# Optimization experiments

Measured on AMD Instinct MI355X. Metric: run time of the kernel, lower is better.

## Reference

```python
import jax, jax.numpy as jnp
import numpy as np

L, B, S, H, V = 6, 8, 2048, 768, 32000
FF = 4 * H
EPS = 1e-5


def _ln(x, g, b):
    m = x.mean(-1, keepdims=True)
    v = ((x - m) ** 2).mean(-1, keepdims=True)
    return (x - m) / jnp.sqrt(v + EPS) * g + b


def setup_inputs() -> dict:
    key = jax.random.key(0)
    ks = iter(jax.random.split(key, 32))
    std = 0.02
    n = lambda shape: jax.random.normal(next(ks), shape, dtype=jnp.float32) * std
    inp = {
        'input_ids': jax.random.randint(next(ks), (B, S), 0, V, dtype=jnp.int64),
        'attention_mask': jnp.ones((B, S), dtype=jnp.int32),
        'tok_emb': n((V, H)),
        'pos_emb': n((S, H)),
        'Wq': n((L, H, H)), 'bq': n((L, H)),
        'Wk': n((L, H, H)), 'bk': n((L, H)),
        'Wv': n((L, H, H)), 'bv': n((L, H)),
        'Wo': n((L, H, H)), 'bo': n((L, H)),
        'ln1_g': jnp.ones((L, H), jnp.float32), 'ln1_b': jnp.zeros((L, H), jnp.float32),
        'ln2_g': jnp.ones((L, H), jnp.float32), 'ln2_b': jnp.zeros((L, H), jnp.float32),
        'W1': n((L, H, FF)), 'b1': n((L, FF)),
        'W2': n((L, FF, H)), 'b2': n((L, H)),
        'fln_g': jnp.ones((H,), jnp.float32), 'fln_b': jnp.zeros((H,), jnp.float32),
        'cls_W': n((H, 1)), 'cls_b': n((1,)),
    }
    return inp


def reference(input_ids, attention_mask, tok_emb, pos_emb, Wq, bq, Wk, bk, Wv, bv,
              Wo, bo, ln1_g, ln1_b, ln2_g, ln2_b, W1, b1, W2, b2,
              fln_g, fln_b, cls_W, cls_b):
    x = tok_emb[input_ids] + pos_emb[None, :S, :]  # [B,S,H]
    causal = jnp.triu(jnp.ones((S, S), dtype=bool), 1)  # True above diagonal
    pad = ~(attention_mask.astype(bool))[:, None, :]    # [B,1,S] True where padded
    full_mask = causal[None, :, :] | pad                # [B,S,S]
    scale = 1.0 / (H ** 0.5)
    for i in range(L):
        # --- attention block (pre-LN) ---
        h = _ln(x, ln1_g[i], ln1_b[i])
        q = h @ Wq[i] + bq[i]
        k = h @ Wk[i] + bk[i]
        v = h @ Wv[i] + bv[i]
        scores = jnp.einsum('bqd,bkd->bqk', q, k) * scale
        scores = jnp.where(full_mask, -jnp.inf, scores)
        attn = jax.nn.softmax(scores, axis=-1)
        o = jnp.einsum('bqk,bkd->bqd', attn, v) @ Wo[i] + bo[i]
        x = o + x
        # --- FFN block ---
        h = _ln(x, ln2_g[i], ln2_b[i])
        x = jax.nn.gelu(h @ W1[i] + b1[i], approximate=False) @ W2[i] + b2[i] + x
    x = _ln(x, fln_g, fln_b)
    # select hidden state of last non-padded token per row
    m = attention_mask.astype(jnp.int32)
    last = m.sum(1) - 1                      # [B]
    x_last = x[jnp.arange(B), last]          # [B,H]
    logits = x_last @ cls_W + cls_b          # [B,1]
    return logits
```

## Files before the change

kernel.cpp:

```cpp
#include <hip/hip_runtime.h>
#include <hip/hip_bf16.h>

#define Bn 8
#define Sn 2048
#define Hn 768
#define FFn 3072
#define Ln 6
#define BSn (Bn * Sn)
#define CQ 512
#define LN_EPS 1e-5f

typedef __hip_bfloat16 bf16;
typedef __bf16 bf16x8 __attribute__((ext_vector_type(8)));
typedef float f32x4 __attribute__((ext_vector_type(4)));

__device__ __forceinline__ float b2f(bf16 v) { return __bfloat162float(v); }
__device__ __forceinline__ void stc(float* p, float v) { *p = v; }
__device__ __forceinline__ void stc(bf16* p, float v) { *p = __float2bfloat16(v); }

union Pk8 { float4 v; bf16 h[8]; };

__device__ __forceinline__ void gld16(const bf16* g, short* l) {
  __builtin_amdgcn_global_load_lds(
      (const __attribute__((address_space(1))) unsigned int*)g,
      (__attribute__((address_space(3))) unsigned int*)l, 16, 0, 0);
}

__global__ void __launch_bounds__(256) embed_kernel(
    const int* __restrict__ ids, const float* __restrict__ tok,
    const float* __restrict__ pos, float* __restrict__ x) {
  long t = blockIdx.x;
  int s = (int)(t & (Sn - 1));
  long id = ids[t];
  const float* tr = tok + id * Hn;
  const float* pr = pos + (long)s * Hn;
  float* xr = x + t * Hn;
  for (int d = threadIdx.x; d < Hn; d += 256)
    xr[d] = tr[d] + pr[d];
}

__global__ void __launch_bounds__(256) transpose_all_kernel(
    const float* __restrict__ Wq_l, const float* __restrict__ Wk_l,
    const float* __restrict__ Wv_l, const float* __restrict__ Wo_l,
    const float* __restrict__ W1_l, const float* __restrict__ W2_l,
    bf16* __restrict__ wt) {
  int id = blockIdx.x;
  const float* W;
  bf16* Wt;
  int K, N, tile, tilesX;
  if (id < 2304) {
    int w = id / 576;
    tile = id - w * 576;
    W = (w == 0) ? Wq_l : (w == 1) ? Wk_l : (w == 2) ? Wv_l : Wo_l;
    Wt = wt + (size_t)w * Hn * Hn;
    K = Hn; N = Hn; tilesX = Hn / 32;
  } else if (id < 4608) {
    tile = id - 2304;
    W = W1_l;
    Wt = wt + 4 * (size_t)Hn * Hn;
    K = Hn; N = FFn; tilesX = FFn / 32;
  } else {
    tile = id - 4608;
    W = W2_l;
    Wt = wt + 4 * (size_t)Hn * Hn + (size_t)Hn * FFn;
    K = FFn; N = Hn; tilesX = Hn / 32;
  }
  int n0 = (tile % tilesX) * 32, k0 = (tile / tilesX) * 32;

  __shared__ float t[32][33];
  int tx = threadIdx.x & 31, ty = threadIdx.x >> 5;
#pragma unroll
  for (int i = 0; i < 32; i += 8)
    t[ty + i][tx] = W[(long)(k0 + ty + i) * N + n0 + tx];
  __syncthreads();
#pragma unroll
  for (int i = 0; i < 32; i += 8)
    stc(Wt + (long)(n0 + ty + i) * K + k0 + tx, t[tx][ty + i]);
}

__global__ void __launch_bounds__(256) ln_kernel(
    const float* __restrict__ x, const float* __restrict__ g,
    const float* __restrict__ b, bf16* __restrict__ out) {
  long token = blockIdx.x;
  const float* xr = x + token * Hn;
  bf16* orow = out + token * Hn;
  int tid = threadIdx.x;

  float vals[3];
  float s1 = 0.f;
#pragma unroll
  for (int i = 0; i < 3; i++) {
    vals[i] = xr[tid + 256 * i];
    s1 += vals[i];
  }
  __shared__ float sb[4];
  __shared__ float stat[2];
#pragma unroll
  for (int off = 32; off > 0; off >>= 1) s1 += __shfl_down(s1, off, 64);
  if ((tid & 63) == 0) sb[tid >> 6] = s1;
  __syncthreads();
  if (tid == 0) stat[0] = (sb[0] + sb[1] + sb[2] + sb[3]) * (1.0f / Hn);
  __syncthreads();
  float mean = stat[0];

  float s2 = 0.f;
#pragma unroll
  for (int i = 0; i < 3; i++) {
    float d = vals[i] - mean;
    s2 += d * d;
  }
#pragma unroll
  for (int off = 32; off > 0; off >>= 1) s2 += __shfl_down(s2, off, 64);
  if ((tid & 63) == 0) sb[tid >> 6] = s2;
  __syncthreads();
  if (tid == 0)
    stat[1] = rsqrtf((sb[0] + sb[1] + sb[2] + sb[3]) * (1.0f / Hn) + LN_EPS);
  __syncthreads();
  float inv = stat[1];

#pragma unroll
  for (int i = 0; i < 3; i++) {
    int d = tid + 256 * i;
    stc(orow + d, (vals[i] - mean) * inv * g[d] + b[d]);
  }
}

template <int EPI, typename CT>
__global__ void __launch_bounds__(256) mfma_gemm_kernel(
    const bf16* __restrict__ A, const bf16* __restrict__ Bt,
    const float* __restrict__ bias, const float* __restrict__ res,
    CT* __restrict__ C, int M, int N, int K,
    const float* __restrict__ bias2, const float* __restrict__ bias3) {
  __shared__ short As[128 * 32];
  __shared__ short Bs[128 * 32];
  int tid = threadIdx.x;
  int wave = tid >> 6, lane = tid & 63;
  int waveM = wave >> 1, waveN = wave & 1;
  int quad = lane >> 4, l16 = lane & 15;

  int nwg = gridDim.x;
  int orig = blockIdx.x;
  int q8 = nwg >> 3, r8 = nwg & 7;
  int xcd = orig & 7, loc = orig >> 3;
  int wg = (xcd < r8 ? xcd * (q8 + 1) : r8 * (q8 + 1) + (xcd - r8) * q8) + loc;
  int gx = N >> 7;
  long colBase = (long)(wg % gx) * 128;
  long rowBase = (long)(wg / gx) * 128;

  const bf16* Ag = A + rowBase * K;
  const bf16* Bg = Bt + colBase * K;

  int srow = lane >> 2;
  int schunk = (lane & 3) * 8;

  f32x4 acc[4][4] = {};

  for (int kt = 0; kt < K; kt += 32) {
#pragma unroll
    for (int c = 0; c < 2; c++) {
      int r0 = wave * 32 + c * 16;
      gld16(Ag + (long)(r0 + srow) * K + kt + schunk, &As[r0 * 32]);
      gld16(Bg + (long)(r0 + srow) * K + kt + schunk, &Bs[r0 * 32]);
    }
    __syncthreads();

    bf16x8 af[4], bfr[4];
#pragma unroll
    for (int t = 0; t < 4; t++)
      af[t] = *(const bf16x8*)&As[(waveM * 64 + t * 16 + l16) * 32 + quad * 8];
#pragma unroll
    for (int u = 0; u < 4; u++)
      bfr[u] = *(const bf16x8*)&Bs[(waveN * 64 + u * 16 + l16) * 32 + quad * 8];
#pragma unroll
    for (int t = 0; t < 4; t++)
#pragma unroll
      for (int u = 0; u < 4; u++)
        acc[t][u] = __builtin_amdgcn_mfma_f32_16x16x32_bf16(af[t], bfr[u],
                                                            acc[t][u], 0, 0, 0);
    __syncthreads();
  }

#pragma unroll
  for (int t = 0; t < 4; t++) {
#pragma unroll
    for (int u = 0; u < 4; u++) {
      int col = (int)colBase + waveN * 64 + u * 16 + l16;
      if (EPI == 4) {
        long row0 = rowBase + waveM * 64 + t * 16 + quad * 4;
        if (col < 1536) {
          float bv = col < 768 ? bias[col] : bias2[col - 768];
          bf16* dst = (bf16*)C + (col < 768 ? 0 : (size_t)BSn * Hn - Hn);
#pragma unroll
          for (int r = 0; r < 4; r++)
            stc(dst + (row0 + r) * Hn + col, acc[t][u][r] + bv);
        } else {
          int vcol = col - 1536;
          float bv = bias3[vcol];
          union { uint2 w; bf16 h[4]; } pk;
          long bb = row0 >> 11;
          long s = row0 & (Sn - 1);
#pragma unroll
          for (int r = 0; r < 4; r++)
            pk.h[r] = __float2bfloat16(acc[t][u][r] + bv);
          bf16* vT = (bf16*)C + 2 * (size_t)BSn * Hn;
          *reinterpret_cast<uint2*>(vT + (bb * Hn + vcol) * Sn + s) = pk.w;
        }
      } else {
        float bv = bias[col];
#pragma unroll
        for (int r = 0; r < 4; r++) {
          long row = rowBase + waveM * 64 + t * 16 + quad * 4 + r;
          float v = acc[t][u][r] + bv;
          if (EPI == 1) v += res[row * N + col];
          if (EPI == 2) v = 0.5f * v * (1.0f + erff(v * 0.70710678118654752f));
          stc(C + row * N + col, v);
        }
      }
    }
  }
}

__global__ void __launch_bounds__(256) qk_mfma_kernel(
    const bf16* __restrict__ q, const bf16* __restrict__ k,
    bf16* __restrict__ sc, int q0) {
  int kBase = blockIdx.x * 128;
  int qBase = q0 + blockIdx.y * 128;
  if (kBase > qBase + 127) return;
  int b = blockIdx.z;
  const bf16* Ag = q + ((long)b * Sn + qBase) * Hn;
  const bf16* Bg = k + ((long)b * Sn + kBase) * Hn;

  __shared__ short As[128 * 32];
  __shared__ short Bs[128 * 32];
  int tid = threadIdx.x;
  int wave = tid >> 6, lane = tid & 63;
  int waveM = wave >> 1, waveN = wave & 1;
  int quad = lane >> 4, l16 = lane & 15;
  int srow = lane >> 2;
  int schunk = (lane & 3) * 8;

  f32x4 acc[4][4] = {};

  for (int kt = 0; kt < Hn; kt += 32) {
#pragma unroll
    for (int c = 0; c < 2; c++) {
      int r0 = wave * 32 + c * 16;
      gld16(Ag + (long)(r0 + srow) * Hn + kt + schunk, &As[r0 * 32]);
      gld16(Bg + (long)(r0 + srow) * Hn + kt + schunk, &Bs[r0 * 32]);
    }
    __syncthreads();

    bf16x8 af[4], bfr[4];
#pragma unroll
    for (int t = 0; t < 4; t++)
      af[t] = *(const bf16x8*)&As[(waveM * 64 + t * 16 + l16) * 32 + quad * 8];
#pragma unroll
    for (int u = 0; u < 4; u++)
      bfr[u] = *(const bf16x8*)&Bs[(waveN * 64 + u * 16 + l16) * 32 + quad * 8];
#pragma unroll
    for (int t = 0; t < 4; t++)
#pragma unroll
      for (int u = 0; u < 4; u++)
        acc[t][u] = __builtin_amdgcn_mfma_f32_16x16x32_bf16(af[t], bfr[u],
                                                            acc[t][u], 0, 0, 0);
    __syncthreads();
  }

  const float scale = 0.03608439182435161f;
#pragma unroll
  for (int t = 0; t < 4; t++)
#pragma unroll
    for (int u = 0; u < 4; u++) {
      int col = kBase + waveN * 64 + u * 16 + l16;
#pragma unroll
      for (int r = 0; r < 4; r++) {
        long qRel = (long)(qBase - q0) + waveM * 64 + t * 16 + quad * 4 + r;
        stc(sc + ((long)b * CQ + qRel) * Sn + col, acc[t][u][r] * scale);
      }
    }
}

__global__ void __launch_bounds__(256) pv_mfma_kernel(
    const bf16* __restrict__ p, const bf16* __restrict__ vT,
    bf16* __restrict__ o, int q0) {
  int colBase = blockIdx.x * 128;
  int qBase = q0 + blockIdx.y * 128;
  int b = blockIdx.z;
  int klimit = qBase + 128;
  const bf16* Ag = p + ((long)b * CQ + (qBase - q0)) * Sn;
  const bf16* Bg = vT + ((long)b * Hn + colBase) * Sn;

  __shared__ short As[128 * 32];
  __shared__ short Bs[128 * 32];
  int tid = threadIdx.x;
  int wave = tid >> 6, lane = tid & 63;
  int waveM = wave >> 1, waveN = wave & 1;
  int quad = lane >> 4, l16 = lane & 15;
  int srow = lane >> 2;
  int schunk = (lane & 3) * 8;

  f32x4 acc[4][4] = {};

  for (int kt = 0; kt < klimit; kt += 32) {
#pragma unroll
    for (int c = 0; c < 2; c++) {
      int r0 = wave * 32 + c * 16;
      gld16(Ag + (long)(r0 + srow) * Sn + kt + schunk, &As[r0 * 32]);
      gld16(Bg + (long)(r0 + srow) * Sn + kt + schunk, &Bs[r0 * 32]);
    }
    __syncthreads();

    bf16x8 af[4], bfr[4];
#pragma unroll
    for (int t = 0; t < 4; t++)
      af[t] = *(const bf16x8*)&As[(waveM * 64 + t * 16 + l16) * 32 + quad * 8];
#pragma unroll
    for (int u = 0; u < 4; u++)
      bfr[u] = *(const bf16x8*)&Bs[(waveN * 64 + u * 16 + l16) * 32 + quad * 8];
#pragma unroll
    for (int t = 0; t < 4; t++)
#pragma unroll
      for (int u = 0; u < 4; u++)
        acc[t][u] = __builtin_amdgcn_mfma_f32_16x16x32_bf16(af[t], bfr[u],
                                                            acc[t][u], 0, 0, 0);
    __syncthreads();
  }

#pragma unroll
  for (int t = 0; t < 4; t++)
#pragma unroll
    for (int u = 0; u < 4; u++) {
      int col = colBase + waveN * 64 + u * 16 + l16;
#pragma unroll
      for (int r = 0; r < 4; r++) {
        long qAbs = (long)qBase + waveM * 64 + t * 16 + quad * 4 + r;
        stc(o + ((long)b * Sn + qAbs) * Hn + col, acc[t][u][r]);
      }
    }
}

__global__ void __launch_bounds__(256) softmax_kernel(
    bf16* __restrict__ sc, const int* __restrict__ mask, int q0) {
  int qRel = blockIdx.x;
  int b = blockIdx.y;
  int qg = q0 + qRel;
  bf16* row = sc + ((long)b * CQ + qRel) * Sn;
  const int* mrow = mask + b * Sn;
  int tid = threadIdx.x;
  int n = qg + 1;
  int limit = (qg & ~127) + 128;
  int k0 = tid * 8;

  Pk8 pk;
  pk.v = *reinterpret_cast<const float4*>(row + k0);
  int4 m0 = *reinterpret_cast<const int4*>(mrow + k0);
  int4 m1 = *reinterpret_cast<const int4*>(mrow + k0 + 4);
  int mm[8] = {m0.x, m0.y, m0.z, m0.w, m1.x, m1.y, m1.z, m1.w};

  float sv[8];
  float lmax = -1e30f;
#pragma unroll
  for (int j = 0; j < 8; j++) {
    int kk = k0 + j;
    float s = (kk < n && mm[j] != 0) ? b2f(pk.h[j]) : -1e30f;
    sv[j] = s;
    lmax = fmaxf(lmax, s);
  }
  __shared__ float sb[4];
  __shared__ float stat;
#pragma unroll
  for (int off = 32; off > 0; off >>= 1)
    lmax = fmaxf(lmax, __shfl_down(lmax, off, 64));
  if ((tid & 63) == 0) sb[tid >> 6] = lmax;
  __syncthreads();
  if (tid == 0) stat = fmaxf(fmaxf(sb[0], sb[1]), fmaxf(sb[2], sb[3]));
  __syncthreads();
  float gmax = stat;

  float ev[8];
  float lsum = 0.f;
#pragma unroll
  for (int j = 0; j < 8; j++) {
    float e = (sv[j] > -1e29f) ? __expf(sv[j] - gmax) : 0.f;
    ev[j] = e;
    lsum += e;
  }
#pragma unroll
  for (int off = 32; off > 0; off >>= 1) lsum += __shfl_down(lsum, off, 64);
  if ((tid & 63) == 0) sb[tid >> 6] = lsum;
  __syncthreads();
  if (tid == 0) stat = sb[0] + sb[1] + sb[2] + sb[3];
  __syncthreads();
  float inv = 1.0f / stat;

  if (k0 < limit) {
    Pk8 o;
#pragma unroll
    for (int j = 0; j < 8; j++)
      o.h[j] = __float2bfloat16((k0 + j < n) ? ev[j] * inv : 0.f);
    *reinterpret_cast<float4*>(row + k0) = o.v;
  }
}

__global__ void __launch_bounds__(256) cls_kernel(
    const bf16* __restrict__ h, const int* __restrict__ mask,
    const float* __restrict__ clsW, const float* __restrict__ clsb,
    float* __restrict__ out) {
  int b = blockIdx.x;
  int tid = threadIdx.x;
  __shared__ float sb[4];
  __shared__ int ib[4];
  __shared__ int lastsh;

  int ls = 0;
  for (int s = tid; s < Sn; s += 256) ls += mask[b * Sn + s];
#pragma unroll
  for (int off = 32; off > 0; off >>= 1) ls += __shfl_down(ls, off, 64);
  if ((tid & 63) == 0) ib[tid >> 6] = ls;
  __syncthreads();
  if (tid == 0) lastsh = ib[0] + ib[1] + ib[2] + ib[3] - 1;
  __syncthreads();
  int last = lastsh;

  const bf16* row = h + ((long)b * Sn + last) * Hn;
  float acc = 0.f;
  for (int d = tid; d < Hn; d += 256) acc += b2f(row[d]) * clsW[d];
#pragma unroll
  for (int off = 32; off > 0; off >>= 1) acc += __shfl_down(acc, off, 64);
  if ((tid & 63) == 0) sb[tid >> 6] = acc;
  __syncthreads();
  if (tid == 0) out[b] = sb[0] + sb[1] + sb[2] + sb[3] + clsb[0];
}

extern "C" void kernel_launch(void* const* d_in, const int* in_sizes, int n_in,
                              void* d_out, int out_size, void* d_ws,
                              size_t ws_size, hipStream_t stream) {
  const int* ids     = (const int*)d_in[0];
  const int* mask    = (const int*)d_in[1];
  const float* tok   = (const float*)d_in[2];
  const float* pos   = (const float*)d_in[3];
  const float* Wq    = (const float*)d_in[4];
  const float* bq    = (const float*)d_in[5];
  const float* Wk    = (const float*)d_in[6];
  const float* bk    = (const float*)d_in[7];
  const float* Wv    = (const float*)d_in[8];
  const float* bv    = (const float*)d_in[9];
  const float* Wo    = (const float*)d_in[10];
  const float* bo    = (const float*)d_in[11];
  const float* ln1g  = (const float*)d_in[12];
  const float* ln1b  = (const float*)d_in[13];
  const float* ln2g  = (const float*)d_in[14];
  const float* ln2b  = (const float*)d_in[15];
  const float* W1    = (const float*)d_in[16];
  const float* b1    = (const float*)d_in[17];
  const float* W2    = (const float*)d_in[18];
  const float* b2    = (const float*)d_in[19];
  const float* flng  = (const float*)d_in[20];
  const float* flnb  = (const float*)d_in[21];
  const float* clsW  = (const float*)d_in[22];
  const float* clsb  = (const float*)d_in[23];

  float* x = (float*)d_ws;
  bf16* h  = (bf16*)(x + (size_t)BSn * Hn);
  bf16* cb = h + (size_t)BSn * Hn;
  bf16* qb = cb;
  bf16* kb = cb + (size_t)BSn * Hn;
  bf16* vtb = cb + 2 * (size_t)BSn * Hn;
  bf16* scb = cb + 3 * (size_t)BSn * Hn;
  bf16* wt = cb + (size_t)BSn * FFn;
  bf16* wqT = wt;
  bf16* woT = wqT + 3 * (size_t)Hn * Hn;
  bf16* w1T = woT + (size_t)Hn * Hn;
  bf16* w2T = w1T + (size_t)Hn * FFn;

  const int M = BSn;
  dim3 blk(256);
  dim3 gridQKV(3 * 2304 / 3);
  dim3 gridH1((Hn / 128) * (M / 128));
  dim3 gridF1((FFn / 128) * (M / 128));
  dim3 gridQK(Sn / 128, CQ / 128, Bn);
  dim3 gridSM(CQ, Bn);
  dim3 gridPV(Hn / 128, CQ / 128, Bn);

  embed_kernel<<<BSn, blk, 0, stream>>>(ids, tok, pos, x);

  for (int l = 0; l < Ln; l++) {
    const float* Wq_l = Wq + (size_t)l * Hn * Hn;
    const float* Wk_l = Wk + (size_t)l * Hn * Hn;
    const float* Wv_l = Wv + (size_t)l * Hn * Hn;
    const float* Wo_l = Wo + (size_t)l * Hn * Hn;
    const float* W1_l = W1 + (size_t)l * Hn * FFn;
    const float* W2_l = W2 + (size_t)l * FFn * Hn;

    transpose_all_kernel<<<6912, blk, 0, stream>>>(Wq_l, Wk_l, Wv_l, Wo_l,
                                                   W1_l, W2_l, wt);

    ln_kernel<<<BSn, blk, 0, stream>>>(x, ln1g + l * Hn, ln1b + l * Hn, h);
    mfma_gemm_kernel<4, bf16><<<dim3(18 * (M / 128)), blk, 0, stream>>>(
        h, wqT, bq + l * Hn, nullptr, qb, M, 3 * Hn, Hn,
        bk + l * Hn, bv + l * Hn);
    for (int c = 0; c < Sn / CQ; c++) {
      int q0 = c * CQ;
      qk_mfma_kernel<<<gridQK, blk, 0, stream>>>(qb, kb, scb, q0);
      softmax_kernel<<<gridSM, blk, 0, stream>>>(scb, mask, q0);
      pv_mfma_kernel<<<gridPV, blk, 0, stream>>>(scb, vtb, h, q0);
    }
    mfma_gemm_kernel<1, float><<<gridH1, blk, 0, stream>>>(
        h, woT, bo + l * Hn, x, x, M, Hn, Hn, nullptr, nullptr);

    ln_kernel<<<BSn, blk, 0, stream>>>(x, ln2g + l * Hn, ln2b + l * Hn, h);
    mfma_gemm_kernel<2, bf16><<<gridF1, blk, 0, stream>>>(
        h, w1T, b1 + l * FFn, nullptr, cb, M, FFn, Hn, nullptr, nullptr);
    mfma_gemm_kernel<1, float><<<gridH1, blk, 0, stream>>>(
        cb, w2T, b2 + l * Hn, x, x, M, Hn, FFn, nullptr, nullptr);
  }

  ln_kernel<<<BSn, blk, 0, stream>>>(x, flng, flnb, h);
  cls_kernel<<<Bn, blk, 0, stream>>>(h, mask, clsW, clsb, (float*)d_out);
}
```

Before: 4.439 ms.

## Replace dense GEMMs with 256x256-tile double-buffered swizzled-LDS MFMA kernel

Replaces the 128x128, 256-thread projection/FFN GEMM with a 256x256 tile, 512-thread kernel that uses a 64-wide K step, double-buffered LDS with an XOR swizzle, and interleaved prefetch of the next stages alongside four MFMA phases raised with setprio. It is meant to increase data reuse per tile, reduce LDS bank conflicts, and hide global-load latency behind compute. In exchange it uses 128KB of LDS per block and launches fewer workgroups (192 for the N=768 GEMMs), which may underfill the GPU. Manual waitcnt and barrier scheduling adds correctness risk.

```diff
diff --git a/kernel.cpp b/kernel.cpp
--- a/kernel.cpp
+++ b/kernel.cpp
@@ -25,6 +25,14 @@
       (const __attribute__((address_space(1))) unsigned int*)g,
       (__attribute__((address_space(3))) unsigned int*)l, 16, 0, 0);
 }
+
+#define BAR() __builtin_amdgcn_s_barrier()
+#define LGKM0()                                            \
+  {                                                        \
+    asm volatile("s_waitcnt lgkmcnt(0)" ::: "memory");     \
+    __builtin_amdgcn_sched_barrier(0);                     \
+  }
+#define VMC(n) asm volatile("s_waitcnt vmcnt(" #n ")" ::: "memory")
 
 __global__ void __launch_bounds__(256) embed_kernel(
     const int* __restrict__ ids, const float* __restrict__ tok,
@@ -126,73 +134,117 @@
 }
 
 template <int EPI, typename CT>
-__global__ void __launch_bounds__(256) mfma_gemm_kernel(
+__global__ void __launch_bounds__(512) gemm256_kernel(
     const bf16* __restrict__ A, const bf16* __restrict__ Bt,
     const float* __restrict__ bias, const float* __restrict__ res,
     CT* __restrict__ C, int M, int N, int K,
     const float* __restrict__ bias2, const float* __restrict__ bias3) {
-  __shared__ short As[128 * 32];
-  __shared__ short Bs[128 * 32];
+  __shared__ short lds[65536];
   int tid = threadIdx.x;
   int wave = tid >> 6, lane = tid & 63;
-  int waveM = wave >> 1, waveN = wave & 1;
+  int wm = wave >> 2, wn = wave & 3;
   int quad = lane >> 4, l16 = lane & 15;
-
-  int nwg = gridDim.x;
-  int orig = blockIdx.x;
+  int swz = (l16 & 7) << 4;
+  int g = lane >> 3;
+  int kswz = ((lane & 7) ^ g) * 8;
+
+  int nwg = gridDim.x, orig = blockIdx.x;
   int q8 = nwg >> 3, r8 = nwg & 7;
   int xcd = orig & 7, loc = orig >> 3;
   int wg = (xcd < r8 ? xcd * (q8 + 1) : r8 * (q8 + 1) + (xcd - r8) * q8) + loc;
-  int gx = N >> 7;
-  long colBase = (long)(wg % gx) * 128;
-  long rowBase = (long)(wg / gx) * 128;
+  int gx = N >> 8;
+  long colBase = (long)(wg % gx) * 256;
+  long rowBase = (long)(wg / gx) * 256;
 
   const bf16* Ag = A + rowBase * K;
   const bf16* Bg = Bt + colBase * K;
 
-  int srow = lane >> 2;
-  int schunk = (lane & 3) * 8;
-
-  f32x4 acc[4][4] = {};
-
-  for (int kt = 0; kt < K; kt += 32) {
-#pragma unroll
-    for (int c = 0; c < 2; c++) {
-      int r0 = wave * 32 + c * 16;
-      gld16(Ag + (long)(r0 + srow) * K + kt + schunk, &As[r0 * 32]);
-      gld16(Bg + (long)(r0 + srow) * K + kt + schunk, &Bs[r0 * 32]);
-    }
-    __syncthreads();
-
-    bf16x8 af[4], bfr[4];
-#pragma unroll
-    for (int t = 0; t < 4; t++)
-      af[t] = *(const bf16x8*)&As[(waveM * 64 + t * 16 + l16) * 32 + quad * 8];
-#pragma unroll
-    for (int u = 0; u < 4; u++)
-      bfr[u] = *(const bf16x8*)&Bs[(waveN * 64 + u * 16 + l16) * 32 + quad * 8];
-#pragma unroll
-    for (int t = 0; t < 4; t++)
-#pragma unroll
-      for (int u = 0; u < 4; u++)
-        acc[t][u] = __builtin_amdgcn_mfma_f32_16x16x32_bf16(af[t], bfr[u],
-                                                            acc[t][u], 0, 0, 0);
-    __syncthreads();
-  }
-
-#pragma unroll
-  for (int t = 0; t < 4; t++) {
-#pragma unroll
-    for (int u = 0; u < 4; u++) {
-      int col = (int)colBase + waveN * 64 + u * 16 + l16;
+  f32x4 acc[8][4] = {};
+  bf16x8 af[4][2], bfr[2][2][2];
+
+#define STAGEA(T, odd)                                                     \
+  {                                                                        \
+    short* base_ = lds + ((T) & 1) * 32768;                                \
+    long kt_ = (long)(T) * 64;                                             \
+    _Pragma("unroll") for (int j_ = 0; j_ < 2; j_++) {                     \
+      int c_ = wave * 2 + j_;                                              \
+      int r0_ = (odd) * 64 + ((c_ >> 3) << 7) + ((c_ & 7) << 3);           \
+      gld16(Ag + (long)(r0_ + g) * K + kt_ + kswz, base_ + r0_ * 64);      \
+    }                                                                      \
+  }
+#define STAGEB(T, odd)                                                     \
+  {                                                                        \
+    short* base_ = lds + ((T) & 1) * 32768 + 16384;                        \
+    long kt_ = (long)(T) * 64;                                             \
+    _Pragma("unroll") for (int j_ = 0; j_ < 2; j_++) {                     \
+      int c_ = wave * 2 + j_;                                              \
+      int r0_ = (odd) * 32 + ((c_ >> 2) << 6) + ((c_ & 3) << 3);           \
+      gld16(Bg + (long)(r0_ + g) * K + kt_ + kswz, base_ + r0_ * 64);      \
+    }                                                                      \
+  }
+#define LOADA(T, h)                                                        \
+  {                                                                        \
+    const char* base_ = (const char*)(lds + ((T) & 1) * 32768);            \
+    _Pragma("unroll") for (int i_ = 0; i_ < 4; i_++) {                     \
+      const char* rp_ = base_ + (wm * 128 + (h) * 64 + i_ * 16 + l16) * 128; \
+      _Pragma("unroll") for (int s_ = 0; s_ < 2; s_++)                     \
+          af[i_][s_] = *(const bf16x8*)(rp_ + ((s_ * 64 + quad * 16) ^ swz)); \
+    }                                                                      \
+  }
+#define LOADB(T, nh)                                                       \
+  {                                                                        \
+    const char* base_ = (const char*)(lds + ((T) & 1) * 32768 + 16384);    \
+    _Pragma("unroll") for (int j_ = 0; j_ < 2; j_++) {                     \
+      const char* rp_ = base_ + (wn * 64 + (nh) * 32 + j_ * 16 + l16) * 128; \
+      _Pragma("unroll") for (int s_ = 0; s_ < 2; s_++)                     \
+          bfr[nh][j_][s_] = *(const bf16x8*)(rp_ + ((s_ * 64 + quad * 16) ^ swz)); \
+    }                                                                      \
+  }
+#define MFMA_PH(h, nh)                                                     \
+  __builtin_amdgcn_s_setprio(1);                                           \
+  _Pragma("unroll") for (int i_ = 0; i_ < 4; i_++)                         \
+      _Pragma("unroll") for (int j_ = 0; j_ < 2; j_++)                     \
+          _Pragma("unroll") for (int s_ = 0; s_ < 2; s_++)                 \
+              acc[(h) * 4 + i_][(nh) * 2 + j_] =                           \
+                  __builtin_amdgcn_mfma_f32_16x16x32_bf16(                 \
+                      af[i_][s_], bfr[nh][j_][s_],                         \
+                      acc[(h) * 4 + i_][(nh) * 2 + j_], 0, 0, 0);          \
+  __builtin_amdgcn_s_setprio(0);
+
+  int NT = K >> 6;
+  STAGEA(0, 0); STAGEB(0, 0); STAGEB(0, 1); STAGEA(0, 1);
+  STAGEA(1, 0); STAGEB(1, 0); STAGEB(1, 1);
+  VMC(6);
+  BAR();
+
+  for (int T = 0; T < NT; T++) {
+    LOADA(T, 0); LOADB(T, 0);
+    if (T + 1 < NT) STAGEA(T + 1, 1);
+    BAR(); LGKM0(); MFMA_PH(0, 0); BAR();
+    LOADB(T, 1);
+    if (T + 2 < NT) STAGEA(T + 2, 0);
+    BAR(); LGKM0(); MFMA_PH(0, 1); BAR();
+    LOADA(T, 1);
+    if (T + 2 < NT) STAGEB(T + 2, 0);
+    BAR(); LGKM0(); MFMA_PH(1, 1); BAR();
+    if (T + 2 < NT) { STAGEB(T + 2, 1); VMC(6); }
+    else { VMC(0); }
+    BAR(); MFMA_PH(1, 0); BAR();
+  }
+
+#pragma unroll
+  for (int mi = 0; mi < 8; mi++) {
+#pragma unroll
+    for (int nj = 0; nj < 4; nj++) {
+      int col = (int)colBase + wn * 64 + nj * 16 + l16;
+      long row0 = rowBase + wm * 128 + mi * 16 + quad * 4;
       if (EPI == 4) {
-        long row0 = rowBase + waveM * 64 + t * 16 + quad * 4;
         if (col < 1536) {
           float bv = col < 768 ? bias[col] : bias2[col - 768];
           bf16* dst = (bf16*)C + (col < 768 ? 0 : (size_t)BSn * Hn - Hn);
 #pragma unroll
           for (int r = 0; r < 4; r++)
-            stc(dst + (row0 + r) * Hn + col, acc[t][u][r] + bv);
+            stc(dst + (row0 + r) * Hn + col, acc[mi][nj][r] + bv);
         } else {
           int vcol = col - 1536;
           float bv = bias3[vcol];
@@ -201,7 +253,7 @@
           long s = row0 & (Sn - 1);
 #pragma unroll
           for (int r = 0; r < 4; r++)
-            pk.h[r] = __float2bfloat16(acc[t][u][r] + bv);
+            pk.h[r] = __float2bfloat16(acc[mi][nj][r] + bv);
           bf16* vT = (bf16*)C + 2 * (size_t)BSn * Hn;
           *reinterpret_cast<uint2*>(vT + (bb * Hn + vcol) * Sn + s) = pk.w;
         }
@@ -209,8 +261,8 @@
         float bv = bias[col];
 #pragma unroll
         for (int r = 0; r < 4; r++) {
-          long row = rowBase + waveM * 64 + t * 16 + quad * 4 + r;
-          float v = acc[t][u][r] + bv;
+          long row = row0 + r;
+          float v = acc[mi][nj][r] + bv;
           if (EPI == 1) v += res[row * N + col];
           if (EPI == 2) v = 0.5f * v * (1.0f + erff(v * 0.70710678118654752f));
           stc(C + row * N + col, v);
@@ -218,6 +270,11 @@
       }
     }
   }
+#undef STAGEA
+#undef STAGEB
+#undef LOADA
+#undef LOADB
+#undef MFMA_PH
 }
 
 __global__ void __launch_bounds__(256) qk_mfma_kernel(
@@ -250,18 +307,18 @@
     }
     __syncthreads();
 
-    bf16x8 af[4], bfr[4];
+    bf16x8 af[4], bfrg[4];
 #pragma unroll
     for (int t = 0; t < 4; t++)
       af[t] = *(const bf16x8*)&As[(waveM * 64 + t * 16 + l16) * 32 + quad * 8];
 #pragma unroll
     for (int u = 0; u < 4; u++)
-      bfr[u] = *(const bf16x8*)&Bs[(waveN * 64 + u * 16 + l16) * 32 + quad * 8];
+      bfrg[u] = *(const bf16x8*)&Bs[(waveN * 64 + u * 16 + l16) * 32 + quad * 8];
 #pragma unroll
     for (int t = 0; t < 4; t++)
 #pragma unroll
       for (int u = 0; u < 4; u++)
-        acc[t][u] = __builtin_amdgcn_mfma_f32_16x16x32_bf16(af[t], bfr[u],
+        acc[t][u] = __builtin_amdgcn_mfma_f32_16x16x32_bf16(af[t], bfrg[u],
                                                             acc[t][u], 0, 0, 0);
     __syncthreads();
   }
@@ -310,18 +367,18 @@
     }
     __syncthreads();
 
-    bf16x8 af[4], bfr[4];
+    bf16x8 af[4], bfrg[4];
 #pragma unroll
     for (int t = 0; t < 4; t++)
       af[t] = *(const bf16x8*)&As[(waveM * 64 + t * 16 + l16) * 32 + quad * 8];
 #pragma unroll
     for (int u = 0; u < 4; u++)
-      bfr[u] = *(const bf16x8*)&Bs[(waveN * 64 + u * 16 + l16) * 32 + quad * 8];
+      bfrg[u] = *(const bf16x8*)&Bs[(waveN * 64 + u * 16 + l16) * 32 + quad * 8];
 #pragma unroll
     for (int t = 0; t < 4; t++)
 #pragma unroll
       for (int u = 0; u < 4; u++)
-        acc[t][u] = __builtin_amdgcn_mfma_f32_16x16x32_bf16(af[t], bfr[u],
+        acc[t][u] = __builtin_amdgcn_mfma_f32_16x16x32_bf16(af[t], bfrg[u],
                                                             acc[t][u], 0, 0, 0);
     __syncthreads();
   }
@@ -475,9 +532,7 @@
 
   const int M = BSn;
   dim3 blk(256);
-  dim3 gridQKV(3 * 2304 / 3);
-  dim3 gridH1((Hn / 128) * (M / 128));
-  dim3 gridF1((FFn / 128) * (M / 128));
+  dim3 blk512(512);
   dim3 gridQK(Sn / 128, CQ / 128, Bn);
   dim3 gridSM(CQ, Bn);
   dim3 gridPV(Hn / 128, CQ / 128, Bn);
@@ -496,7 +551,7 @@
                                                    W1_l, W2_l, wt);
 
     ln_kernel<<<BSn, blk, 0, stream>>>(x, ln1g + l * Hn, ln1b + l * Hn, h);
-    mfma_gemm_kernel<4, bf16><<<dim3(18 * (M / 128)), blk, 0, stream>>>(
+    gemm256_kernel<4, bf16><<<576, blk512, 0, stream>>>(
         h, wqT, bq + l * Hn, nullptr, qb, M, 3 * Hn, Hn,
         bk + l * Hn, bv + l * Hn);
     for (int c = 0; c < Sn / CQ; c++) {
@@ -505,13 +560,13 @@
       softmax_kernel<<<gridSM, blk, 0, stream>>>(scb, mask, q0);
       pv_mfma_kernel<<<gridPV, blk, 0, stream>>>(scb, vtb, h, q0);
     }
-    mfma_gemm_kernel<1, float><<<gridH1, blk, 0, stream>>>(
+    gemm256_kernel<1, float><<<192, blk512, 0, stream>>>(
         h, woT, bo + l * Hn, x, x, M, Hn, Hn, nullptr, nullptr);
 
     ln_kernel<<<BSn, blk, 0, stream>>>(x, ln2g + l * Hn, ln2b + l * Hn, h);
-    mfma_gemm_kernel<2, bf16><<<gridF1, blk, 0, stream>>>(
+    gemm256_kernel<2, bf16><<<768, blk512, 0, stream>>>(
         h, w1T, b1 + l * FFn, nullptr, cb, M, FFn, Hn, nullptr, nullptr);
-    mfma_gemm_kernel<1, float><<<gridH1, blk, 0, stream>>>(
+    gemm256_kernel<1, float><<<192, blk512, 0, stream>>>(
         cb, w2T, b2 + l * Hn, x, x, M, Hn, FFn, nullptr, nullptr);
   }
 
```

Result: faster. 4.001 ms (-9.9%).

## Double-buffer GEMM LDS tiles with XOR swizzle and polynomial GELU

Applied to the files above, without the earlier changes.

Reworks the dense GEMM kernel into a two-stage double-buffered pipeline: the next K-tile is issued via global_load_lds while MFMAs run on the current buffer. An XOR swizzle on the LDS layout is meant to avoid bank conflicts, and s_setprio raises wave priority around the MFMA block. The exact erff GELU is replaced by an Abramowitz-Stegun polynomial approximation, which is cheaper but slightly less accurate. Launch bounds now request 4 waves per SIMD occupancy, and LDS use doubles to 32KB per block.

```diff
diff --git a/kernel.cpp b/kernel.cpp
--- a/kernel.cpp
+++ b/kernel.cpp
@@ -24,6 +24,21 @@
   __builtin_amdgcn_global_load_lds(
       (const __attribute__((address_space(1))) unsigned int*)g,
       (__attribute__((address_space(3))) unsigned int*)l, 16, 0, 0);
+}
+
+#define BAR() __builtin_amdgcn_s_barrier()
+#define VMC(n) asm volatile("s_waitcnt vmcnt(" #n ")" ::: "memory")
+
+__device__ __forceinline__ float gelu_exact(float v) {
+  float a = fabsf(v) * 0.70710678118654752f;
+  float t = 1.0f / (1.0f + 0.3275911f * a);
+  float poly = t * (0.254829592f +
+               t * (-0.284496736f +
+               t * (1.421413741f +
+               t * (-1.453152027f + t * 1.061405429f))));
+  float er = 1.0f - poly * __expf(-a * a);
+  er = v < 0.f ? -er : er;
+  return 0.5f * v * (1.0f + er);
 }
 
 __global__ void __launch_bounds__(256) embed_kernel(
@@ -126,20 +141,21 @@
 }
 
 template <int EPI, typename CT>
-__global__ void __launch_bounds__(256) mfma_gemm_kernel(
+__global__ void __launch_bounds__(256, 4) gemm128_kernel(
     const bf16* __restrict__ A, const bf16* __restrict__ Bt,
     const float* __restrict__ bias, const float* __restrict__ res,
     CT* __restrict__ C, int M, int N, int K,
     const float* __restrict__ bias2, const float* __restrict__ bias3) {
-  __shared__ short As[128 * 32];
-  __shared__ short Bs[128 * 32];
+  __shared__ short lds[16384];
   int tid = threadIdx.x;
   int wave = tid >> 6, lane = tid & 63;
-  int waveM = wave >> 1, waveN = wave & 1;
+  int wm = wave >> 1, wn = wave & 1;
   int quad = lane >> 4, l16 = lane & 15;
-
-  int nwg = gridDim.x;
-  int orig = blockIdx.x;
+  int swz = (l16 & 3) << 4;
+  int g = lane >> 2;
+  int kswz = ((lane & 3) ^ (g & 3)) * 8;
+
+  int nwg = gridDim.x, orig = blockIdx.x;
   int q8 = nwg >> 3, r8 = nwg & 7;
   int xcd = orig & 7, loc = orig >> 3;
   int wg = (xcd < r8 ? xcd * (q8 + 1) : r8 * (q8 + 1) + (xcd - r8) * q8) + loc;
@@ -147,52 +163,69 @@
   long colBase = (long)(wg % gx) * 128;
   long rowBase = (long)(wg / gx) * 128;
 
-  const bf16* Ag = A + rowBase * K;
-  const bf16* Bg = Bt + colBase * K;
-
-  int srow = lane >> 2;
-  int schunk = (lane & 3) * 8;
+  const bf16* aSrc = A + rowBase * K + (long)g * K + kswz;
+  const bf16* bSrc = Bt + colBase * K + (long)g * K + kswz;
+
+  int r0A0 = wave * 32, r0A1 = wave * 32 + 16;
+  long sA0 = (long)r0A0 * K, sA1 = (long)r0A1 * K;
+
+  char* lb = (char*)lds;
+  const char* aRd = lb + (wm * 64 + l16) * 64 + ((quad * 16) ^ swz);
+  const char* bRd = lb + 8192 + (wn * 64 + l16) * 64 + ((quad * 16) ^ swz);
 
   f32x4 acc[4][4] = {};
-
-  for (int kt = 0; kt < K; kt += 32) {
-#pragma unroll
-    for (int c = 0; c < 2; c++) {
-      int r0 = wave * 32 + c * 16;
-      gld16(Ag + (long)(r0 + srow) * K + kt + schunk, &As[r0 * 32]);
-      gld16(Bg + (long)(r0 + srow) * K + kt + schunk, &Bs[r0 * 32]);
-    }
-    __syncthreads();
-
-    bf16x8 af[4], bfr[4];
-#pragma unroll
-    for (int t = 0; t < 4; t++)
-      af[t] = *(const bf16x8*)&As[(waveM * 64 + t * 16 + l16) * 32 + quad * 8];
-#pragma unroll
-    for (int u = 0; u < 4; u++)
-      bfr[u] = *(const bf16x8*)&Bs[(waveN * 64 + u * 16 + l16) * 32 + quad * 8];
-#pragma unroll
-    for (int t = 0; t < 4; t++)
-#pragma unroll
-      for (int u = 0; u < 4; u++)
-        acc[t][u] = __builtin_amdgcn_mfma_f32_16x16x32_bf16(af[t], bfr[u],
-                                                            acc[t][u], 0, 0, 0);
-    __syncthreads();
-  }
-
-#pragma unroll
-  for (int t = 0; t < 4; t++) {
-#pragma unroll
-    for (int u = 0; u < 4; u++) {
-      int col = (int)colBase + waveN * 64 + u * 16 + l16;
+  bf16x8 af[4], bfr[4];
+
+#define STAGE(BUF, KOFF)                                                    \
+  {                                                                         \
+    gld16(aSrc + sA0 + (KOFF), (short*)(lb + (BUF) * 16384 + r0A0 * 64));   \
+    gld16(aSrc + sA1 + (KOFF), (short*)(lb + (BUF) * 16384 + r0A1 * 64));   \
+    gld16(bSrc + sA0 + (KOFF),                                              \
+          (short*)(lb + (BUF) * 16384 + 8192 + r0A0 * 64));                 \
+    gld16(bSrc + sA1 + (KOFF),                                              \
+          (short*)(lb + (BUF) * 16384 + 8192 + r0A1 * 64));                 \
+  }
+#define COMPUTE(BUF)                                                        \
+  {                                                                         \
+    _Pragma("unroll") for (int i_ = 0; i_ < 4; i_++)                        \
+        af[i_] = *(const bf16x8*)(aRd + (BUF) * 16384 + i_ * 1024);         \
+    _Pragma("unroll") for (int j_ = 0; j_ < 4; j_++)                        \
+        bfr[j_] = *(const bf16x8*)(bRd + (BUF) * 16384 + j_ * 1024);        \
+    __builtin_amdgcn_s_setprio(1);                                          \
+    _Pragma("unroll") for (int i_ = 0; i_ < 4; i_++)                        \
+        _Pragma("unroll") for (int j_ = 0; j_ < 4; j_++)                    \
+            acc[i_][j_] = __builtin_amdgcn_mfma_f32_16x16x32_bf16(          \
+                af[i_], bfr[j_], acc[i_][j_], 0, 0, 0);                     \
+    __builtin_amdgcn_s_setprio(0);                                          \
+  }
+
+  int NT = K >> 5;
+  STAGE(0, 0);
+  VMC(0); BAR();
+
+  for (int T = 0; T < NT; T += 2) {
+    STAGE(1, 32);
+    COMPUTE(0);
+    VMC(0); BAR();
+    if (T + 2 < NT) STAGE(0, 64);
+    COMPUTE(1);
+    VMC(0); BAR();
+    aSrc += 64; bSrc += 64;
+  }
+
+#pragma unroll
+  for (int mi = 0; mi < 4; mi++) {
+#pragma unroll
+    for (int nj = 0; nj < 4; nj++) {
+      int col = (int)colBase + wn * 64 + nj * 16 + l16;
+      long row0 = rowBase + wm * 64 + mi * 16 + quad * 4;
       if (EPI == 4) {
-        long row0 = rowBase + waveM * 64 + t * 16 + quad * 4;
         if (col < 1536) {
           float bv = col < 768 ? bias[col] : bias2[col - 768];
           bf16* dst = (bf16*)C + (col < 768 ? 0 : (size_t)BSn * Hn - Hn);
 #pragma unroll
           for (int r = 0; r < 4; r++)
-            stc(dst + (row0 + r) * Hn + col, acc[t][u][r] + bv);
+            stc(dst + (row0 + r) * Hn + col, acc[mi][nj][r] + bv);
         } else {
           int vcol = col - 1536;
           float bv = bias3[vcol];
@@ -201,7 +234,7 @@
           long s = row0 & (Sn - 1);
 #pragma unroll
           for (int r = 0; r < 4; r++)
-            pk.h[r] = __float2bfloat16(acc[t][u][r] + bv);
+            pk.h[r] = __float2bfloat16(acc[mi][nj][r] + bv);
           bf16* vT = (bf16*)C + 2 * (size_t)BSn * Hn;
           *reinterpret_cast<uint2*>(vT + (bb * Hn + vcol) * Sn + s) = pk.w;
         }
@@ -209,15 +242,17 @@
         float bv = bias[col];
 #pragma unroll
         for (int r = 0; r < 4; r++) {
-          long row = rowBase + waveM * 64 + t * 16 + quad * 4 + r;
-          float v = acc[t][u][r] + bv;
+          long row = row0 + r;
+          float v = acc[mi][nj][r] + bv;
           if (EPI == 1) v += res[row * N + col];
-          if (EPI == 2) v = 0.5f * v * (1.0f + erff(v * 0.70710678118654752f));
+          if (EPI == 2) v = gelu_exact(v);
           stc(C + row * N + col, v);
         }
       }
     }
   }
+#undef STAGE
+#undef COMPUTE
 }
 
 __global__ void __launch_bounds__(256) qk_mfma_kernel(
@@ -250,18 +285,18 @@
     }
     __syncthreads();
 
-    bf16x8 af[4], bfr[4];
+    bf16x8 af[4], bfrg[4];
 #pragma unroll
     for (int t = 0; t < 4; t++)
       af[t] = *(const bf16x8*)&As[(waveM * 64 + t * 16 + l16) * 32 + quad * 8];
 #pragma unroll
     for (int u = 0; u < 4; u++)
-      bfr[u] = *(const bf16x8*)&Bs[(waveN * 64 + u * 16 + l16) * 32 + quad * 8];
+      bfrg[u] = *(const bf16x8*)&Bs[(waveN * 64 + u * 16 + l16) * 32 + quad * 8];
 #pragma unroll
     for (int t = 0; t < 4; t++)
 #pragma unroll
       for (int u = 0; u < 4; u++)
-        acc[t][u] = __builtin_amdgcn_mfma_f32_16x16x32_bf16(af[t], bfr[u],
+        acc[t][u] = __builtin_amdgcn_mfma_f32_16x16x32_bf16(af[t], bfrg[u],
                                                             acc[t][u], 0, 0, 0);
     __syncthreads();
   }
@@ -310,18 +345,18 @@
     }
     __syncthreads();
 
-    bf16x8 af[4], bfr[4];
+    bf16x8 af[4], bfrg[4];
 #pragma unroll
     for (int t = 0; t < 4; t++)
       af[t] = *(const bf16x8*)&As[(waveM * 64 + t * 16 + l16) * 32 + quad * 8];
 #pragma unroll
     for (int u = 0; u < 4; u++)
-      bfr[u] = *(const bf16x8*)&Bs[(waveN * 64 + u * 16 + l16) * 32 + quad * 8];
+      bfrg[u] = *(const bf16x8*)&Bs[(waveN * 64 + u * 16 + l16) * 32 + quad * 8];
 #pragma unroll
     for (int t = 0; t < 4; t++)
 #pragma unroll
       for (int u = 0; u < 4; u++)
-        acc[t][u] = __builtin_amdgcn_mfma_f32_16x16x32_bf16(af[t], bfr[u],
+        acc[t][u] = __builtin_amdgcn_mfma_f32_16x16x32_bf16(af[t], bfrg[u],
                                                             acc[t][u], 0, 0, 0);
     __syncthreads();
   }
@@ -475,9 +510,6 @@
 
   const int M = BSn;
   dim3 blk(256);
-  dim3 gridQKV(3 * 2304 / 3);
-  dim3 gridH1((Hn / 128) * (M / 128));
-  dim3 gridF1((FFn / 128) * (M / 128));
   dim3 gridQK(Sn / 128, CQ / 128, Bn);
   dim3 gridSM(CQ, Bn);
   dim3 gridPV(Hn / 128, CQ / 128, Bn);
@@ -496,7 +528,7 @@
                                                    W1_l, W2_l, wt);
 
     ln_kernel<<<BSn, blk, 0, stream>>>(x, ln1g + l * Hn, ln1b + l * Hn, h);
-    mfma_gemm_kernel<4, bf16><<<dim3(18 * (M / 128)), blk, 0, stream>>>(
+    gemm128_kernel<4, bf16><<<2304, blk, 0, stream>>>(
         h, wqT, bq + l * Hn, nullptr, qb, M, 3 * Hn, Hn,
         bk + l * Hn, bv + l * Hn);
     for (int c = 0; c < Sn / CQ; c++) {
@@ -505,13 +537,13 @@
       softmax_kernel<<<gridSM, blk, 0, stream>>>(scb, mask, q0);
       pv_mfma_kernel<<<gridPV, blk, 0, stream>>>(scb, vtb, h, q0);
     }
-    mfma_gemm_kernel<1, float><<<gridH1, blk, 0, stream>>>(
+    gemm128_kernel<1, float><<<768, blk, 0, stream>>>(
         h, woT, bo + l * Hn, x, x, M, Hn, Hn, nullptr, nullptr);
 
     ln_kernel<<<BSn, blk, 0, stream>>>(x, ln2g + l * Hn, ln2b + l * Hn, h);
-    mfma_gemm_kernel<2, bf16><<<gridF1, blk, 0, stream>>>(
+    gemm128_kernel<2, bf16><<<3072, blk, 0, stream>>>(
         h, w1T, b1 + l * FFn, nullptr, cb, M, FFn, Hn, nullptr, nullptr);
-    mfma_gemm_kernel<1, float><<<gridH1, blk, 0, stream>>>(
+    gemm128_kernel<1, float><<<768, blk, 0, stream>>>(
         cb, w2T, b2 + l * Hn, x, x, M, Hn, FFn, nullptr, nullptr);
   }
 
```

New measurement: 3.925 ms. 1.13x faster.
